# Kernel tuning notes

Hardware: AMD Instinct MI355X
Metric: run time of the kernel (lower is better)

The kernel has to match this reference:

```python
import jax, jax.numpy as jnp
import numpy as np

NEG_SLOPE = 0.01  # torch nn.LeakyReLU default


def setup_inputs() -> dict:
    key = jax.random.key(0)
    k1, k2, k3 = jax.random.split(key, 3)
    B, H, D, L = 4, 8, 64, 2048
    q = jax.random.normal(k1, (B, H, D, L), dtype=jnp.float32)
    k = jax.random.normal(k2, (B, H, D, L), dtype=jnp.float32)
    v = jax.random.normal(k3, (B, H, D, L), dtype=jnp.float32)
    return {"q": q, "k": k, "v": v}


def reference(q, k, v):
    # q, k, v: [B, H, D, L] (note: feature dim BEFORE length, as in the torch module)
    d_tensor = q.shape[2]
    scale = 1.0 / np.sqrt(d_tensor).astype(np.float32)
    # scores = LeakyReLU(q^T k / sqrt(d)) : [B, H, Lq, Lk]
    scores = jnp.einsum('bhdq,bhdk->bhqk', q, k) * scale
    scores = jax.nn.leaky_relu(scores, negative_slope=NEG_SLOPE)
    psi = jax.nn.softmax(scores, axis=-1)
    # out = (psi @ v^T)^T : [B, H, D, Lq]
    out = jnp.einsum('bhqk,bhdk->bhdq', psi, v)
    return out
```

## Files before the change

kernel.cpp:

```cpp
#include <hip/hip_runtime.h>
#include <math.h>

#define DD 64
#define LL 2048
#define HEADS 32
#define TQ 128
#define TK 64
#define NTHREADS 512
#define QSCALE 0.18033688011112042f

typedef __bf16 bf16_t;
typedef __bf16 bf16x8 __attribute__((ext_vector_type(8)));
typedef float f32x16 __attribute__((ext_vector_type(16)));

__global__ __launch_bounds__(256)
void prep_bf16_kv(const float* __restrict__ k, const float* __restrict__ v,
                  bf16_t* __restrict__ kt, bf16_t* __restrict__ vb) {
  __shared__ float ld[64][65];
  const int t = threadIdx.x;
  const int which = blockIdx.z;
  const int head = blockIdx.y;
  const int l0 = blockIdx.x * 64;
  const size_t hoff = (size_t)head * DD * LL;
  if (which == 1) {
    const float* src = v + hoff;
    bf16_t* dst = vb + hoff;
    const int lp = (t & 31) * 2;
    const int db = (t >> 5) * 8;
    for (int i = 0; i < 8; ++i) {
      int d = db + i;
      float2 x = *(const float2*)(src + (size_t)d * LL + l0 + lp);
      union { bf16_t b[2]; unsigned u; } pk;
      pk.b[0] = (bf16_t)x.x;
      pk.b[1] = (bf16_t)x.y;
      *(unsigned*)(dst + (size_t)d * LL + l0 + lp) = pk.u;
    }
  } else {
    const float* src = k + hoff;
    bf16_t* dst = kt + hoff;
    const int l = t & 63;
    const int db = (t >> 6) * 16;
    for (int i = 0; i < 16; ++i) {
      int d = db + i;
      ld[l][d] = src[(size_t)d * LL + l0 + l];
    }
    __syncthreads();
    const int dp = (t & 31) * 2;
    const int lb = (t >> 5) * 8;
    for (int i = 0; i < 8; ++i) {
      int lw = lb + i;
      union { bf16_t b[2]; unsigned u; } pk;
      pk.b[0] = (bf16_t)ld[lw][dp];
      pk.b[1] = (bf16_t)ld[lw][dp + 1];
      *(unsigned*)(dst + (size_t)(l0 + lw) * DD + dp) = pk.u;
    }
  }
}

struct __align__(16) SMemA4 {
  union {
    bf16_t Qs[TQ][72];
    bf16_t Ks[2][TK][72];
  } qk;
  bf16_t Vs[2][DD][72];
};
union __align__(16) SMemU4 {
  SMemA4 a;
  float Oe[TQ][65];
};

__global__ __launch_bounds__(NTHREADS, 4)
void attn_flash_bf16_v5(const float* __restrict__ q, const bf16_t* __restrict__ kt,
                        const bf16_t* __restrict__ vb, float* __restrict__ out) {
  __shared__ SMemU4 sm;
  __shared__ float rs1[TQ];
  const int tid  = threadIdx.x;
  const int w    = tid >> 6;
  const int lane = tid & 63;
  const int l31  = lane & 31;
  const int hh   = lane >> 5;
  const int strip = w & 3;
  const int half  = w >> 2;
  const int wbase = strip * 32;
  const int lkh   = half * 32;
  const int bid  = blockIdx.x;
  const int j    = bid >> 3;
  const int head = (bid & 7) + 8 * (j >> 4);
  const int q0   = (j & 15) * TQ;
  const size_t hoff = (size_t)head * DD * LL;
  const float*  qp = q  + hoff;
  const bf16_t* kp = kt + hoff;
  const bf16_t* vp = vb + hoff;

  const int srow = tid >> 3;
  const int scol = (tid & 7) * 8;

  bf16x8 kreg = *(const bf16x8*)(kp + (size_t)srow * DD + scol);
  bf16x8 vreg = *(const bf16x8*)(vp + (size_t)srow * LL + scol);

  {
    int lq  = tid & 127;
    int d0q = (tid >> 7) * 16;
    const float* src = qp + q0 + lq;
    for (int g = 0; g < 2; ++g) {
      bf16x8 pk;
      for (int jj = 0; jj < 8; ++jj)
        pk[jj] = (bf16_t)(src[(size_t)(d0q + g * 8 + jj) * LL] * QSCALE);
      *(bf16x8*)&sm.a.qk.Qs[lq][d0q + g * 8] = pk;
    }
  }

  __syncthreads();
  bf16x8 bq[4];
  for (int kk = 0; kk < 4; ++kk)
    bq[kk] = *(const bf16x8*)&sm.a.qk.Qs[wbase + l31][kk * 16 + 8 * hh];
  __syncthreads();

  f32x16 oacc[2];
  for (int dt = 0; dt < 2; ++dt)
    for (int r = 0; r < 16; ++r) oacc[dt][r] = 0.f;
  float rsl[4];
  for (int i = 0; i < 4; ++i) rsl[i] = 0.f;

  for (int t = 0; t < LL / TK; ++t) {
    const int cur = t & 1;
    *(bf16x8*)&sm.a.qk.Ks[cur][srow][scol] = kreg;
    *(bf16x8*)&sm.a.Vs[cur][srow][scol]    = vreg;
    __syncthreads();

    if (t + 1 < LL / TK) {
      const int lk0n = (t + 1) * TK;
      kreg = *(const bf16x8*)(kp + (size_t)(lk0n + srow) * DD + scol);
      vreg = *(const bf16x8*)(vp + (size_t)srow * LL + lk0n + scol);
    }

    f32x16 st;
    for (int r = 0; r < 16; ++r) st[r] = 0.f;
    __builtin_amdgcn_s_setprio(1);
    for (int kk = 0; kk < 4; ++kk) {
      bf16x8 ak = *(const bf16x8*)&sm.a.qk.Ks[cur][lkh + l31][kk * 16 + 8 * hh];
      st = __builtin_amdgcn_mfma_f32_32x32x16_bf16(ak, bq[kk], st, 0, 0, 0);
    }
    __builtin_amdgcn_s_setprio(0);

    unsigned pb[8];
#pragma unroll
    for (int r = 0; r < 16; ++r) {
      float s = st[r];
      s = fmaxf(s, 0.01f * s);
      float p = __builtin_amdgcn_exp2f(s);
      rsl[r & 3] += p;
      st[r] = p;
    }
    for (int qq = 0; qq < 8; ++qq) {
      union { bf16_t b[2]; unsigned u; } pk;
      pk.b[0] = (bf16_t)st[2 * qq];
      pk.b[1] = (bf16_t)st[2 * qq + 1];
      pb[qq] = pk.u;
    }

    for (int kk2 = 0; kk2 < 2; ++kk2) {
      unsigned l0 = pb[4 * kk2 + 0], l1 = pb[4 * kk2 + 1];
      unsigned l2 = pb[4 * kk2 + 2], l3 = pb[4 * kk2 + 3];
      unsigned s0 = hh ? l0 : l2;
      unsigned s1 = hh ? l1 : l3;
      unsigned f0 = (unsigned)__shfl_xor((int)s0, 32);
      unsigned f1 = (unsigned)__shfl_xor((int)s1, 32);
      union { unsigned u[4]; bf16x8 v; } ap;
      ap.u[0] = hh ? f0 : l0;
      ap.u[1] = hh ? f1 : l1;
      ap.u[2] = hh ? l2 : f0;
      ap.u[3] = hh ? l3 : f1;
      const int lkb = lkh + kk2 * 16 + 8 * hh;
      __builtin_amdgcn_s_setprio(1);
      for (int dt = 0; dt < 2; ++dt) {
        bf16x8 bv = *(const bf16x8*)&sm.a.Vs[cur][dt * 32 + l31][lkb];
        oacc[dt] = __builtin_amdgcn_mfma_f32_32x32x16_bf16(ap.v, bv, oacc[dt], 0, 0, 0);
      }
      __builtin_amdgcn_s_setprio(0);
    }
  }

  float rsum = (rsl[0] + rsl[1]) + (rsl[2] + rsl[3]);
  float rtot = rsum + __shfl_xor(rsum, 32);
  __syncthreads();
  if (half == 1) {
    rs1[wbase + l31] = rtot;
    for (int r = 0; r < 16; ++r) {
      int row = (r & 3) + 8 * (r >> 2) + 4 * hh;
      for (int dt = 0; dt < 2; ++dt)
        sm.Oe[wbase + row][dt * 32 + l31] = oacc[dt][r];
    }
  }
  __syncthreads();
  if (half == 0) {
    float tot = rtot + rs1[wbase + l31];
    rs1[wbase + l31] = 1.0f / tot;
    float inv[16];
    for (int r = 0; r < 16; ++r) {
      int row = (r & 3) + 8 * (r >> 2) + 4 * hh;
      inv[r] = rs1[wbase + row];
    }
    for (int r = 0; r < 16; ++r) {
      int row = (r & 3) + 8 * (r >> 2) + 4 * hh;
      for (int dt = 0; dt < 2; ++dt) {
        int col = dt * 32 + l31;
        sm.Oe[wbase + row][col] = (oacc[dt][r] + sm.Oe[wbase + row][col]) * inv[r];
      }
    }
  }
  __syncthreads();
  float* op = out + hoff + q0;
  for (int i = 0; i < 16; ++i) {
    int idx = tid + NTHREADS * i;
    int d   = idx >> 7;
    int lq  = idx & 127;
    op[(size_t)d * LL + lq] = sm.Oe[lq][d];
  }
}

struct __align__(16) SMemA {
  bf16_t Qs[TQ][72];
  bf16_t Ks[TK][72];
  bf16_t Vs[DD][72];
};
union __align__(16) SMemU {
  SMemA a;
  float Oe[TQ][65];
};

__global__ __launch_bounds__(NTHREADS, 4)
void attn_flash_bf16(const float* __restrict__ q, const float* __restrict__ k,
                     const float* __restrict__ v, float* __restrict__ out) {
  __shared__ SMemU sm;
  __shared__ float rs1[TQ];
  const int tid  = threadIdx.x;
  const int w    = tid >> 6;
  const int lane = tid & 63;
  const int l31  = lane & 31;
  const int hh   = lane >> 5;
  const int strip = w & 3;
  const int half  = w >> 2;
  const int wbase = strip * 32;
  const int lkh   = half * 32;
  const int head = blockIdx.y;
  const int q0   = blockIdx.x * TQ;
  const size_t hoff = (size_t)head * DD * LL;
  const float* qp = q + hoff;
  const float* kp = k + hoff;
  const float* vp = v + hoff;

  {
    int lq  = tid & 127;
    int d0q = (tid >> 7) * 16;
    const float* src = qp + q0 + lq;
    for (int g = 0; g < 2; ++g) {
      bf16x8 pk;
      for (int jj = 0; jj < 8; ++jj)
        pk[jj] = (bf16_t)(src[(size_t)(d0q + g * 8 + jj) * LL] * QSCALE);
      *(bf16x8*)&sm.a.Qs[lq][d0q + g * 8] = pk;
    }
  }

  const int klk = tid & 63;
  const int kd0 = (tid >> 6) * 8;
  const int vd  = tid >> 3;
  const int vc8 = (tid & 7) * 8;

  float  kreg[8];
  float4 vreg[2];
  {
    const float* ks = kp + klk;
    for (int jj = 0; jj < 8; ++jj) kreg[jj] = ks[(size_t)(kd0 + jj) * LL];
    vreg[0] = *(const float4*)(vp + (size_t)vd * LL + vc8);
    vreg[1] = *(const float4*)(vp + (size_t)vd * LL + vc8 + 4);
  }

  __syncthreads();
  bf16x8 bq[4];
  for (int kk = 0; kk < 4; ++kk)
    bq[kk] = *(const bf16x8*)&sm.a.Qs[wbase + l31][kk * 16 + 8 * hh];

  f32x16 oacc[2];
  for (int dt = 0; dt < 2; ++dt)
    for (int r = 0; r < 16; ++r) oacc[dt][r] = 0.f;
  float rsum = 0.f;

  for (int t = 0; t < LL / TK; ++t) {
    __syncthreads();
    {
      bf16x8 pk;
      for (int jj = 0; jj < 8; ++jj) pk[jj] = (bf16_t)kreg[jj];
      *(bf16x8*)&sm.a.Ks[klk][kd0] = pk;
      bf16x8 pv;
      pv[0] = (bf16_t)vreg[0].x; pv[1] = (bf16_t)vreg[0].y;
      pv[2] = (bf16_t)vreg[0].z; pv[3] = (bf16_t)vreg[0].w;
      pv[4] = (bf16_t)vreg[1].x; pv[5] = (bf16_t)vreg[1].y;
      pv[6] = (bf16_t)vreg[1].z; pv[7] = (bf16_t)vreg[1].w;
      *(bf16x8*)&sm.a.Vs[vd][vc8] = pv;
    }
    __syncthreads();

    if (t + 1 < LL / TK) {
      const int lk0n = (t + 1) * TK;
      const float* ks = kp + lk0n + klk;
      for (int jj = 0; jj < 8; ++jj) kreg[jj] = ks[(size_t)(kd0 + jj) * LL];
      vreg[0] = *(const float4*)(vp + (size_t)vd * LL + lk0n + vc8);
      vreg[1] = *(const float4*)(vp + (size_t)vd * LL + lk0n + vc8 + 4);
    }

    f32x16 st;
    for (int r = 0; r < 16; ++r) st[r] = 0.f;
    for (int kk = 0; kk < 4; ++kk) {
      bf16x8 ak = *(const bf16x8*)&sm.a.Ks[lkh + l31][kk * 16 + 8 * hh];
      st = __builtin_amdgcn_mfma_f32_32x32x16_bf16(ak, bq[kk], st, 0, 0, 0);
    }

    unsigned pb[8];
    for (int r = 0; r < 16; ++r) {
      float s = st[r];
      s = fmaxf(s, 0.01f * s);
      float p = __builtin_amdgcn_exp2f(s);
      rsum += p;
      st[r] = p;
    }
    for (int qq = 0; qq < 8; ++qq) {
      union { bf16_t b[2]; unsigned u; } pk;
      pk.b[0] = (bf16_t)st[2 * qq];
      pk.b[1] = (bf16_t)st[2 * qq + 1];
      pb[qq] = pk.u;
    }

    for (int kk2 = 0; kk2 < 2; ++kk2) {
      unsigned l0 = pb[4 * kk2 + 0], l1 = pb[4 * kk2 + 1];
      unsigned l2 = pb[4 * kk2 + 2], l3 = pb[4 * kk2 + 3];
      unsigned s0 = hh ? l0 : l2;
      unsigned s1 = hh ? l1 : l3;
      unsigned f0 = (unsigned)__shfl_xor((int)s0, 32);
      unsigned f1 = (unsigned)__shfl_xor((int)s1, 32);
      union { unsigned u[4]; bf16x8 v; } ap;
      ap.u[0] = hh ? f0 : l0;
      ap.u[1] = hh ? f1 : l1;
      ap.u[2] = hh ? l2 : f0;
      ap.u[3] = hh ? l3 : f1;
      const int lkb = lkh + kk2 * 16 + 8 * hh;
      for (int dt = 0; dt < 2; ++dt) {
        bf16x8 bv = *(const bf16x8*)&sm.a.Vs[dt * 32 + l31][lkb];
        oacc[dt] = __builtin_amdgcn_mfma_f32_32x32x16_bf16(ap.v, bv, oacc[dt], 0, 0, 0);
      }
    }
  }

  float rtot = rsum + __shfl_xor(rsum, 32);
  __syncthreads();
  if (half == 1) {
    rs1[wbase + l31] = rtot;
    for (int r = 0; r < 16; ++r) {
      int row = (r & 3) + 8 * (r >> 2) + 4 * hh;
      for (int dt = 0; dt < 2; ++dt)
        sm.Oe[wbase + row][dt * 32 + l31] = oacc[dt][r];
    }
  }
  __syncthreads();
  if (half == 0) {
    float tot = rtot + rs1[wbase + l31];
    rs1[wbase + l31] = 1.0f / tot;
    float inv[16];
    for (int r = 0; r < 16; ++r) {
      int row = (r & 3) + 8 * (r >> 2) + 4 * hh;
      inv[r] = rs1[wbase + row];
    }
    for (int r = 0; r < 16; ++r) {
      int row = (r & 3) + 8 * (r >> 2) + 4 * hh;
      for (int dt = 0; dt < 2; ++dt) {
        int col = dt * 32 + l31;
        sm.Oe[wbase + row][col] = (oacc[dt][r] + sm.Oe[wbase + row][col]) * inv[r];
      }
    }
  }
  __syncthreads();
  float* op = out + hoff + q0;
  for (int i = 0; i < 16; ++i) {
    int idx = tid + NTHREADS * i;
    int d   = idx >> 7;
    int lq  = idx & 127;
    op[(size_t)d * LL + lq] = sm.Oe[lq][d];
  }
}

extern "C" void kernel_launch(void* const* d_in, const int* in_sizes, int n_in,
                              void* d_out, int out_size, void* d_ws, size_t ws_size,
                              hipStream_t stream) {
  const float* q = (const float*)d_in[0];
  const float* k = (const float*)d_in[1];
  const float* v = (const float*)d_in[2];
  float* out = (float*)d_out;
  const size_t per_buf = (size_t)HEADS * DD * LL;
  const size_t need = 2 * per_buf * sizeof(bf16_t);
  if (d_ws && ws_size >= need) {
    bf16_t* kt = (bf16_t*)d_ws;
    bf16_t* vb = kt + per_buf;
    prep_bf16_kv<<<dim3(LL / 64, HEADS, 2), 256, 0, stream>>>(k, v, kt, vb);
    attn_flash_bf16_v5<<<dim3((LL / TQ) * HEADS), NTHREADS, 0, stream>>>(q, kt, vb, out);
  } else {
    attn_flash_bf16<<<dim3(LL / TQ, HEADS), NTHREADS, 0, stream>>>(q, k, v, out);
  }
}
```

Baseline: 143.9 us.

## Double query tile to 256 with 1024-thread blocks, split K/V staging, permlane32 swap

Result: faster. 139.7 us (-2.9%).

```diff
diff --git a/kernel.cpp b/kernel.cpp
--- a/kernel.cpp
+++ b/kernel.cpp
@@ -5,13 +5,17 @@
 #define LL 2048
 #define HEADS 32
 #define TQ 128
+#define TQ2 256
 #define TK 64
+#define NT (LL / TK)
 #define NTHREADS 512
+#define NTH2 1024
 #define QSCALE 0.18033688011112042f
 
 typedef __bf16 bf16_t;
 typedef __bf16 bf16x8 __attribute__((ext_vector_type(8)));
 typedef float f32x16 __attribute__((ext_vector_type(16)));
+typedef int i32x2 __attribute__((ext_vector_type(2)));
 
 __global__ __launch_bounds__(256)
 void prep_bf16_kv(const float* __restrict__ k, const float* __restrict__ v,
@@ -57,50 +61,56 @@
   }
 }
 
-struct __align__(16) SMemA4 {
+struct __align__(16) SMemA10 {
   union {
-    bf16_t Qs[TQ][72];
-    bf16_t Ks[2][TK][72];
+    bf16_t Qs[TQ2][72];
+    bf16_t Ks[2][64][72];
   } qk;
-  bf16_t Vs[2][DD][72];
+  bf16_t Vs[2][64][72];
 };
-union __align__(16) SMemU4 {
-  SMemA4 a;
-  float Oe[TQ][65];
+union __align__(16) SMemU10 {
+  SMemA10 a;
+  float Oe[TQ2][65];
 };
 
-__global__ __launch_bounds__(NTHREADS, 4)
-void attn_flash_bf16_v5(const float* __restrict__ q, const bf16_t* __restrict__ kt,
-                        const bf16_t* __restrict__ vb, float* __restrict__ out) {
-  __shared__ SMemU4 sm;
-  __shared__ float rs1[TQ];
+__global__ __launch_bounds__(NTH2, 4)
+void attn_flash_bf16_v10(const float* __restrict__ q, const bf16_t* __restrict__ kt,
+                         const bf16_t* __restrict__ vb, float* __restrict__ out) {
+  __shared__ SMemU10 sm;
+  __shared__ float rs1[TQ2];
   const int tid  = threadIdx.x;
   const int w    = tid >> 6;
   const int lane = tid & 63;
   const int l31  = lane & 31;
   const int hh   = lane >> 5;
-  const int strip = w & 3;
-  const int half  = w >> 2;
+  const int strip = w & 7;
+  const int half  = w >> 3;
   const int wbase = strip * 32;
   const int lkh   = half * 32;
   const int bid  = blockIdx.x;
   const int j    = bid >> 3;
-  const int head = (bid & 7) + 8 * (j >> 4);
-  const int q0   = (j & 15) * TQ;
+  const int head = (bid & 7) + 8 * (j >> 3);
+  const int q0   = (j & 7) * TQ2;
   const size_t hoff = (size_t)head * DD * LL;
   const float*  qp = q  + hoff;
   const bf16_t* kp = kt + hoff;
   const bf16_t* vp = vb + hoff;
 
-  const int srow = tid >> 3;
-  const int scol = (tid & 7) * 8;
-
-  bf16x8 kreg = *(const bf16x8*)(kp + (size_t)srow * DD + scol);
-  bf16x8 vreg = *(const bf16x8*)(vp + (size_t)srow * LL + scol);
+  const int sk   = tid >> 9;
+  const int stid = tid & 511;
+  const int srow = stid >> 3;
+  const int scol = (stid & 7) * 8;
+  const bf16_t* sbase = sk ? (vp + (size_t)srow * LL + scol)
+                           : (kp + (size_t)srow * DD + scol);
+  const size_t sstep = sk ? (size_t)TK : (size_t)TK * DD;
+  bf16_t* sdst0 = sk ? &sm.a.Vs[0][srow][scol] : &sm.a.qk.Ks[0][srow][scol];
+  bf16_t* sdst1 = sk ? &sm.a.Vs[1][srow][scol] : &sm.a.qk.Ks[1][srow][scol];
+
+  bf16x8 kvreg = *(const bf16x8*)sbase;
 
   {
-    int lq  = tid & 127;
-    int d0q = (tid >> 7) * 16;
+    int lq  = tid & 255;
+    int d0q = (tid >> 8) * 16;
     const float* src = qp + q0 + lq;
     for (int g = 0; g < 2; ++g) {
       bf16x8 pk;
@@ -122,17 +132,13 @@
   float rsl[4];
   for (int i = 0; i < 4; ++i) rsl[i] = 0.f;
 
-  for (int t = 0; t < LL / TK; ++t) {
+  for (int t = 0; t < NT; ++t) {
     const int cur = t & 1;
-    *(bf16x8*)&sm.a.qk.Ks[cur][srow][scol] = kreg;
-    *(bf16x8*)&sm.a.Vs[cur][srow][scol]    = vreg;
+    *(bf16x8*)(cur ? sdst1 : sdst0) = kvreg;
     __syncthreads();
 
-    if (t + 1 < LL / TK) {
-      const int lk0n = (t + 1) * TK;
-      kreg = *(const bf16x8*)(kp + (size_t)(lk0n + srow) * DD + scol);
-      vreg = *(const bf16x8*)(vp + (size_t)srow * LL + lk0n + scol);
-    }
+    if (t + 1 < NT)
+      kvreg = *(const bf16x8*)(sbase + (size_t)(t + 1) * sstep);
 
     f32x16 st;
     for (int r = 0; r < 16; ++r) st[r] = 0.f;
@@ -160,17 +166,26 @@
     }
 
     for (int kk2 = 0; kk2 < 2; ++kk2) {
-      unsigned l0 = pb[4 * kk2 + 0], l1 = pb[4 * kk2 + 1];
-      unsigned l2 = pb[4 * kk2 + 2], l3 = pb[4 * kk2 + 3];
-      unsigned s0 = hh ? l0 : l2;
-      unsigned s1 = hh ? l1 : l3;
+      unsigned x0 = pb[4 * kk2 + 0], x1 = pb[4 * kk2 + 1];
+      unsigned y0 = pb[4 * kk2 + 2], y1 = pb[4 * kk2 + 3];
+      union { unsigned u[4]; bf16x8 v; } ap;
+#if __has_builtin(__builtin_amdgcn_permlane32_swap)
+      i32x2 r0 = __builtin_amdgcn_permlane32_swap((int)x0, (int)y0, false, false);
+      i32x2 r1 = __builtin_amdgcn_permlane32_swap((int)x1, (int)y1, false, false);
+      ap.u[0] = (unsigned)r0[0];
+      ap.u[1] = (unsigned)r1[0];
+      ap.u[2] = (unsigned)r0[1];
+      ap.u[3] = (unsigned)r1[1];
+#else
+      unsigned s0 = hh ? x0 : y0;
+      unsigned s1 = hh ? x1 : y1;
       unsigned f0 = (unsigned)__shfl_xor((int)s0, 32);
       unsigned f1 = (unsigned)__shfl_xor((int)s1, 32);
-      union { unsigned u[4]; bf16x8 v; } ap;
-      ap.u[0] = hh ? f0 : l0;
-      ap.u[1] = hh ? f1 : l1;
-      ap.u[2] = hh ? l2 : f0;
-      ap.u[3] = hh ? l3 : f1;
+      ap.u[0] = hh ? f0 : x0;
+      ap.u[1] = hh ? f1 : x1;
+      ap.u[2] = hh ? y0 : f0;
+      ap.u[3] = hh ? y1 : f1;
+#endif
       const int lkb = lkh + kk2 * 16 + 8 * hh;
       __builtin_amdgcn_s_setprio(1);
       for (int dt = 0; dt < 2; ++dt) {
@@ -212,9 +227,9 @@
   __syncthreads();
   float* op = out + hoff + q0;
   for (int i = 0; i < 16; ++i) {
-    int idx = tid + NTHREADS * i;
-    int d   = idx >> 7;
-    int lq  = idx & 127;
+    int idx = tid + NTH2 * i;
+    int d   = idx >> 8;
+    int lq  = idx & 255;
     op[(size_t)d * LL + lq] = sm.Oe[lq][d];
   }
 }
@@ -312,8 +327,8 @@
     f32x16 st;
     for (int r = 0; r < 16; ++r) st[r] = 0.f;
     for (int kk = 0; kk < 4; ++kk) {
-      bf16x8 ak = *(const bf16x8*)&sm.a.Ks[lkh + l31][kk * 16 + 8 * hh];
-      st = __builtin_amdgcn_mfma_f32_32x32x16_bf16(ak, bq[kk], st, 0, 0, 0);
+      bf16x8 akf = *(const bf16x8*)&sm.a.Ks[lkh + l31][kk * 16 + 8 * hh];
+      st = __builtin_amdgcn_mfma_f32_32x32x16_bf16(akf, bq[kk], st, 0, 0, 0);
     }
 
     unsigned pb[8];
@@ -345,8 +360,8 @@
       ap.u[3] = hh ? l3 : f1;
       const int lkb = lkh + kk2 * 16 + 8 * hh;
       for (int dt = 0; dt < 2; ++dt) {
-        bf16x8 bv = *(const bf16x8*)&sm.a.Vs[dt * 32 + l31][lkb];
-        oacc[dt] = __builtin_amdgcn_mfma_f32_32x32x16_bf16(ap.v, bv, oacc[dt], 0, 0, 0);
+        bf16x8 bvf = *(const bf16x8*)&sm.a.Vs[dt * 32 + l31][lkb];
+        oacc[dt] = __builtin_amdgcn_mfma_f32_32x32x16_bf16(ap.v, bvf, oacc[dt], 0, 0, 0);
       }
     }
   }
@@ -401,7 +416,7 @@
     bf16_t* kt = (bf16_t*)d_ws;
     bf16_t* vb = kt + per_buf;
     prep_bf16_kv<<<dim3(LL / 64, HEADS, 2), 256, 0, stream>>>(k, v, kt, vb);
-    attn_flash_bf16_v5<<<dim3((LL / TQ) * HEADS), NTHREADS, 0, stream>>>(q, kt, vb, out);
+    attn_flash_bf16_v10<<<dim3((LL / TQ2) * HEADS), NTH2, 0, stream>>>(q, kt, vb, out);
   } else {
     attn_flash_bf16<<<dim3(LL / TQ, HEADS), NTHREADS, 0, stream>>>(q, k, v, out);
   }
```
